# Kernel optimization log

Hardware: AMD Instinct MI355X
Metric: run time of the kernel (lower is better)

## Reference

```python
import jax, jax.numpy as jnp
import numpy as np

NUM_HEADS = 12
KEEP_RATE = 0.7


def setup_inputs() -> dict:
    key = jax.random.key(0)
    ks = jax.random.split(key, 5)
    B, N, C = 64, 197, 768
    x = jax.random.normal(ks[0], (B, N, C), dtype=jnp.float32)
    qkv_w = jax.random.normal(ks[1], (3 * C, C), dtype=jnp.float32) * (C ** -0.5)
    qkv_b = jax.random.normal(ks[2], (3 * C,), dtype=jnp.float32) * 0.02
    proj_w = jax.random.normal(ks[3], (C, C), dtype=jnp.float32) * (C ** -0.5)
    proj_b = jax.random.normal(ks[4], (C,), dtype=jnp.float32) * 0.02
    return {"x": x, "qkv_w": qkv_w, "qkv_b": qkv_b, "proj_w": proj_w, "proj_b": proj_b}


def reference(x, qkv_w, qkv_b, proj_w, proj_b):
    B, N, C = x.shape
    H = NUM_HEADS
    D = C // H
    scale = D ** -0.5
    # qkv projection: [B,N,3C] -> [3,B,H,N,D]
    qkv = (x @ qkv_w.T + qkv_b).reshape(B, N, 3, H, D).transpose(2, 0, 3, 1, 4)
    q, k, v = qkv[0], qkv[1], qkv[2]
    # full materialized attention (required for cls-row extraction)
    attn = jax.nn.softmax(jnp.einsum('bhqd,bhkd->bhqk', q, k) * scale, axis=-1)
    out = jnp.einsum('bhqk,bhkd->bqhd', attn, v).reshape(B, N, C)
    out = out @ proj_w.T + proj_b
    # EViT token pruning: cls-token attention over non-cls keys, head-averaged
    left_tokens = int(KEEP_RATE * (N - 1))  # 137
    cls_attn = attn[:, :, 0, 1:].mean(axis=1)  # [B, N-1]
    _, idx = jax.lax.top_k(cls_attn, left_tokens)  # sorted descending, like torch.topk
    index = jnp.broadcast_to(idx[:, :, None], (B, left_tokens, C))
    return (out, index, idx, cls_attn)
```

## Files before the change

kernel.cpp:

```cpp
#include <hip/hip_runtime.h>
#include <hip/hip_bf16.h>
#include <stdint.h>

constexpr int BATCH = 64;
constexpr int NTOK  = 197;
constexpr int CDIM  = 768;
constexpr int NH    = 12;
constexpr int HD    = 64;
constexpr int MROWS = BATCH * NTOK;
constexpr int MPAD  = 12800;
constexpr int NROWT = MPAD / 128;
constexpr int LEFT  = 137;
constexpr int KPAD  = 224;
constexpr int BH    = BATCH * NH;
constexpr int SPAD  = 208;

constexpr size_t OUT_OFF_OUT   = 0;
constexpr size_t OUT_OFF_INDEX = (size_t)BATCH * NTOK * CDIM;
constexpr size_t OUT_OFF_IDX   = OUT_OFF_INDEX + (size_t)BATCH * LEFT * CDIM;
constexpr size_t OUT_OFF_CLS   = OUT_OFF_IDX + (size_t)BATCH * LEFT;

constexpr size_t WS_CLSPH = 0;
constexpr size_t WS_CLSF  = WS_CLSPH + (size_t)BH * (NTOK - 1);
constexpr size_t WS_IDXI  = WS_CLSF  + (size_t)BATCH * (NTOK - 1);
constexpr size_t WS_Q0    = WS_IDXI  + (size_t)BATCH * LEFT;
constexpr size_t WS_XB    = WS_Q0  + (size_t)BATCH * CDIM;
constexpr size_t WS_WB    = WS_XB  + (size_t)MPAD * CDIM / 2;
constexpr size_t WS_PB    = WS_WB  + (size_t)3 * CDIM * CDIM / 2;
constexpr size_t WS_QB    = WS_PB  + (size_t)CDIM * CDIM / 2;
constexpr size_t WS_KB    = WS_QB  + (size_t)BH * NTOK * HD / 2;
constexpr size_t WS_VTB   = WS_KB  + (size_t)BH * NTOK * HD / 2;
constexpr size_t WS_AOB   = WS_VTB + (size_t)BH * HD * KPAD / 2;
constexpr size_t WS_U     = WS_AOB + (size_t)MPAD * CDIM / 2;
constexpr size_t WS_S     = WS_U   + (size_t)BH * CDIM;

typedef __attribute__((ext_vector_type(8))) short short8;
typedef __attribute__((ext_vector_type(4))) float floatx4;

__device__ __forceinline__ ushort f2bf(float x) {
    __hip_bfloat16 h = __float2bfloat16(x);
    return *(ushort*)&h;
}

__device__ __forceinline__ void load_lds16(const ushort* g, ushort* l) {
    __builtin_amdgcn_global_load_lds(
        (const __attribute__((address_space(1))) uint32_t*)(uintptr_t)g,
        (__attribute__((address_space(3))) uint32_t*)(uint32_t)(uintptr_t)l,
        16, 0, 0);
}

constexpr int X_N4  = MROWS * CDIM / 4;
constexpr int X_NP4 = MPAD * CDIM / 4;
constexpr int W_N4  = 3 * CDIM * CDIM / 4;
constexpr int P_N4  = CDIM * CDIM / 4;
constexpr int CAST_TOTAL = X_NP4 + W_N4 + P_N4;

__global__ __launch_bounds__(256) void cast_all_kernel(const float* __restrict__ x,
                                                       const float* __restrict__ qkv_w,
                                                       const float* __restrict__ proj_w,
                                                       ushort* __restrict__ xb,
                                                       ushort* __restrict__ wb,
                                                       ushort* __restrict__ pb) {
    int i = blockIdx.x * 256 + threadIdx.x;
    const float* src;
    ushort* dst;
    int j, valid;
    if (i < X_NP4) {
        src = x; dst = xb; j = i; valid = (j < X_N4);
    } else if (i < X_NP4 + W_N4) {
        src = qkv_w; dst = wb; j = i - X_NP4; valid = 1;
    } else if (i < CAST_TOTAL) {
        src = proj_w; dst = pb; j = i - X_NP4 - W_N4; valid = 1;
    } else {
        return;
    }
    ushort4 h4 = make_ushort4(0, 0, 0, 0);
    if (valid) {
        float4 a = ((const float4*)src)[j];
        h4 = make_ushort4(f2bf(a.x), f2bf(a.y), f2bf(a.z), f2bf(a.w));
    }
    ((ushort4*)dst)[j] = h4;
}

__global__ __launch_bounds__(256) void q0_kernel(const float* __restrict__ x,
                                                 const float* __restrict__ qkv_w,
                                                 const float* __restrict__ qkv_b,
                                                 float* __restrict__ q0) {
    const int wv   = threadIdx.x >> 6;
    const int lane = threadIdx.x & 63;
    constexpr int CG = CDIM / 4;
    const int b = blockIdx.x / CG;
    const int c = (blockIdx.x - b * CG) * 4 + wv;

    const float* xr = x + (size_t)b * NTOK * CDIM;
    const float* wr = qkv_w + (size_t)c * CDIM;
    float s = 0.f;
#pragma unroll
    for (int i = 0; i < 3; i++) {
        float4 xv = *(const float4*)(xr + lane * 4 + i * 256);
        float4 wv4 = *(const float4*)(wr + lane * 4 + i * 256);
        s += xv.x * wv4.x + xv.y * wv4.y + xv.z * wv4.z + xv.w * wv4.w;
    }
#pragma unroll
    for (int off = 32; off >= 1; off >>= 1) s += __shfl_xor(s, off);
    if (lane == 0) q0[(size_t)b * CDIM + c] = s + qkv_b[c];
}

__global__ __launch_bounds__(256) void u_kernel(const float* __restrict__ q0,
                                                const float* __restrict__ qkv_w,
                                                float* __restrict__ U) {
    const int bh = blockIdx.x;
    const int b  = bh / NH;
    const int h  = bh - b * NH;
    const int t  = threadIdx.x;

    __shared__ float q0s[HD];
    if (t < HD) q0s[t] = q0[(size_t)b * CDIM + h * HD + t];
    __syncthreads();

    const float* wk = qkv_w + (size_t)(CDIM + h * HD) * CDIM;
    float a0 = 0.f, a1 = 0.f, a2 = 0.f;
    for (int d = 0; d < HD; d++) {
        const float qd = q0s[d];
        const float* row = wk + (size_t)d * CDIM;
        a0 = fmaf(qd, row[t],       a0);
        a1 = fmaf(qd, row[t + 256], a1);
        a2 = fmaf(qd, row[t + 512], a2);
    }
    float* ub = U + (size_t)bh * CDIM;
    ub[t] = a0; ub[t + 256] = a1; ub[t + 512] = a2;
}

__global__ __launch_bounds__(256) void score_kernel(const float* __restrict__ x,
                                                    const float* __restrict__ U,
                                                    float* __restrict__ S) {
    const int wv   = threadIdx.x >> 6;
    const int lane = threadIdx.x & 63;
    const int j    = blockIdx.x * 4 + wv;
    const int b    = blockIdx.y;
    if (j >= NTOK) return;

    const float* xr = x + ((size_t)b * NTOK + j) * CDIM;
    float4 xv[3];
#pragma unroll
    for (int i = 0; i < 3; i++) xv[i] = *(const float4*)(xr + lane * 4 + i * 256);

    for (int h = 0; h < NH; h++) {
        const float* ur = U + (size_t)(b * NH + h) * CDIM;
        float s = 0.f;
#pragma unroll
        for (int i = 0; i < 3; i++) {
            float4 uv = *(const float4*)(ur + lane * 4 + i * 256);
            s += xv[i].x * uv.x + xv[i].y * uv.y + xv[i].z * uv.z + xv[i].w * uv.w;
        }
#pragma unroll
        for (int off = 32; off >= 1; off >>= 1) s += __shfl_xor(s, off);
        if (lane == 0) S[(size_t)(b * NH + h) * SPAD + j] = s;
    }
}

template <int MODE, int NCOLT>
__global__ __launch_bounds__(256, 4) void mfma_gemm128(
    const ushort* __restrict__ A, const ushort* __restrict__ W,
    const float* __restrict__ bias,
    float* __restrict__ O0f, ushort* __restrict__ O0q,
    ushort* __restrict__ O1k, ushort* __restrict__ O2vd,
    int Mvalid, int N) {
    constexpr int K   = CDIM;
    constexpr int BK  = 32;
    constexpr int NTK = K / BK;
    __shared__ ushort sA[2 * 128 * BK];
    __shared__ ushort sB[2 * 128 * BK];

    const int t    = threadIdx.x;
    const int lane = t & 63;
    const int w    = t >> 6;
    const int wm   = (w >> 1) * 64;
    const int wn   = (w & 1) * 64;
    const int fr   = lane & 15;
    const int fq   = lane >> 4;
    const int f3   = lane & 3;

    int row, col;
    {
        constexpr int nwg = NROWT * NCOLT;
        constexpr int q = nwg >> 3, r = nwg & 7;
        const int xcd = blockIdx.x & 7, lin = blockIdx.x >> 3;
        const int wg = (xcd < r ? xcd * (q + 1) : r * (q + 1) + (xcd - r) * q) + lin;
        row = wg / NCOLT; col = wg - row * NCOLT;
    }
    const int rowBase = row * 128;
    const int colBase = col * 128;

    auto stage = [&](const ushort* __restrict__ G, ushort* dst, int grow0, int kt) {
#pragma unroll
        for (int i = 0; i < 2; ++i) {
            const int l  = i * 256 + t;
            const int rl = l >> 2;
            const int sl = (l & 3) ^ (rl & 3);
            load_lds16(G + (size_t)(grow0 + rl) * K + kt * BK + sl * 8,
                       dst + l * 8);
        }
    };

    floatx4 acc[4][4];
#pragma unroll
    for (int i = 0; i < 4; ++i)
#pragma unroll
        for (int j = 0; j < 4; ++j)
#pragma unroll
            for (int r2 = 0; r2 < 4; ++r2) acc[i][j][r2] = 0.f;

    const int s0 = (fq ^ f3) * 8;

    stage(A, sA, rowBase, 0);
    stage(W, sB, colBase, 0);

    for (int kt = 0; kt < NTK; ++kt) {
        __syncthreads();
        const int cb = (kt & 1) << 12;
        if (kt + 1 < NTK) {
            stage(A, sA + (cb ^ 4096), rowBase, kt + 1);
            stage(W, sB + (cb ^ 4096), colBase, kt + 1);
        }

        const ushort* pa = sA + cb + (wm + fr) * BK;
        const ushort* pb = sB + cb + (wn + fr) * BK;
        short8 af[4], bf[4];
#pragma unroll
        for (int i = 0; i < 4; ++i) {
            af[i] = *(const short8*)(pa + i * 512 + s0);
            bf[i] = *(const short8*)(pb + i * 512 + s0);
        }
#pragma unroll
        for (int i = 0; i < 4; ++i)
#pragma unroll
            for (int j = 0; j < 4; ++j)
                acc[i][j] = __builtin_amdgcn_mfma_f32_16x16x32_bf16(
                    af[i], bf[j], acc[i][j], 0, 0, 0);
    }

#pragma unroll
    for (int j = 0; j < 4; ++j) {
        const int nn = colBase + wn + j * 16 + fr;
        const float bq = bias[nn];
        if (MODE == 0) {
#pragma unroll
            for (int i = 0; i < 4; ++i) {
                const int mb = rowBase + wm + i * 16 + fq * 4;
#pragma unroll
                for (int r2 = 0; r2 < 4; ++r2) {
                    const int mm = mb + r2;
                    if (mm < Mvalid) O0f[(size_t)mm * N + nn] = acc[i][j][r2] + bq;
                }
            }
        } else {
            const int which = nn / CDIM;
            const int nc    = nn - which * CDIM;
            const int h     = nc >> 6;
            const int d     = nc & 63;
#pragma unroll
            for (int i = 0; i < 4; ++i) {
                const int mb = rowBase + wm + i * 16 + fq * 4;
#pragma unroll
                for (int r2 = 0; r2 < 4; ++r2) {
                    const int mm = mb + r2;
                    if (mm < Mvalid) {
                        const int b   = mm / NTOK;
                        const int tok = mm - b * NTOK;
                        const int bh  = b * NH + h;
                        const ushort val = f2bf(acc[i][j][r2] + bq);
                        if (which == 0)      O0q[((size_t)bh * NTOK + tok) * HD + d] = val;
                        else if (which == 1) O1k[((size_t)bh * NTOK + tok) * HD + d] = val;
                        else                 O2vd[(size_t)mm * CDIM + nc] = val;
                    }
                }
            }
        }
    }
}

__global__ __launch_bounds__(256) void v_transpose_kernel(const ushort* __restrict__ Vd,
                                                          ushort* __restrict__ Vtb) {
    const int bh = blockIdx.x;
    const int b  = bh / NH;
    const int h  = bh - b * NH;
    const int t  = threadIdx.x;

    __shared__ ushort tile[HD][KPAD + 9];

    const int d  = t & 63;
    const int tt = t >> 6;
    const ushort* src = Vd + (size_t)b * NTOK * CDIM + h * HD + d;
    for (int tok0 = 0; tok0 < KPAD; tok0 += 4) {
        const int tok = tok0 + tt;
        ushort v = 0;
        if (tok < NTOK) v = src[(size_t)tok * CDIM];
        tile[d][tok] = v;
    }
    __syncthreads();

    uint* dst = (uint*)(Vtb + (size_t)bh * HD * KPAD);
    constexpr int C2 = KPAD / 2;
    for (int idx = t; idx < HD * C2; idx += 256) {
        const int dd = idx / C2;
        const int c  = idx - dd * C2;
        const uint lo = tile[dd][2 * c];
        const uint hi = tile[dd][2 * c + 1];
        dst[dd * C2 + c] = lo | (hi << 16);
    }
}

__global__ __launch_bounds__(64) void attn_mfma_kernel(const ushort* __restrict__ Qb,
                                                       const ushort* __restrict__ Kb,
                                                       const ushort* __restrict__ Vtb,
                                                       ushort* __restrict__ AOb) {
    const int qt = blockIdx.x;
    const int bh = blockIdx.y;
    const int b  = bh / NH;
    const int h  = bh - b * NH;
    const int lane = threadIdx.x;
    const int qc   = lane & 15;
    const int quad = lane >> 4;

    __shared__ ushort Pl[16][32];
    __shared__ float  alf[16], lf[16];

    const ushort* Qh = Qb  + (size_t)bh * NTOK * HD;
    const ushort* Kh = Kb  + (size_t)bh * NTOK * HD;
    const ushort* Vh = Vtb + (size_t)bh * HD * KPAD;

    const int qrow = min(qt * 16 + qc, NTOK - 1);
    const short8 qf0 = *(const short8*)(Qh + (size_t)qrow * HD + quad * 8);
    const short8 qf1 = *(const short8*)(Qh + (size_t)qrow * HD + 32 + quad * 8);

    floatx4 o[4];
#pragma unroll
    for (int s = 0; s < 4; s++)
#pragma unroll
        for (int r = 0; r < 4; r++) o[s][r] = 0.f;
    float m = -INFINITY, l = 0.f;

    for (int c0 = 0; c0 < NTOK; c0 += 32) {
        const int kr0 = min(c0 + qc, NTOK - 1);
        const int kr1 = min(c0 + 16 + qc, NTOK - 1);
        short8 kf00 = *(const short8*)(Kh + (size_t)kr0 * HD + quad * 8);
        short8 kf01 = *(const short8*)(Kh + (size_t)kr0 * HD + 32 + quad * 8);
        short8 kf10 = *(const short8*)(Kh + (size_t)kr1 * HD + quad * 8);
        short8 kf11 = *(const short8*)(Kh + (size_t)kr1 * HD + 32 + quad * 8);

        floatx4 s0 = {0.f, 0.f, 0.f, 0.f}, s1 = {0.f, 0.f, 0.f, 0.f};
        s0 = __builtin_amdgcn_mfma_f32_16x16x32_bf16(kf00, qf0, s0, 0, 0, 0);
        s0 = __builtin_amdgcn_mfma_f32_16x16x32_bf16(kf01, qf1, s0, 0, 0, 0);
        s1 = __builtin_amdgcn_mfma_f32_16x16x32_bf16(kf10, qf0, s1, 0, 0, 0);
        s1 = __builtin_amdgcn_mfma_f32_16x16x32_bf16(kf11, qf1, s1, 0, 0, 0);

        float sv[8];
        float mloc = -INFINITY;
#pragma unroll
        for (int r = 0; r < 4; r++) {
            const int key0 = c0 + quad * 4 + r;
            const int key1 = key0 + 16;
            sv[r]     = (key0 < NTOK) ? s0[r] * 0.125f : -1e30f;
            sv[4 + r] = (key1 < NTOK) ? s1[r] * 0.125f : -1e30f;
            mloc = fmaxf(mloc, fmaxf(sv[r], sv[4 + r]));
        }
        mloc = fmaxf(mloc, __shfl_xor(mloc, 16));
        mloc = fmaxf(mloc, __shfl_xor(mloc, 32));
        const float mnew  = fmaxf(m, mloc);
        const float alpha = __expf(m - mnew);
        float p[8], ps = 0.f;
#pragma unroll
        for (int i = 0; i < 8; i++) { p[i] = __expf(sv[i] - mnew); ps += p[i]; }
        ps += __shfl_xor(ps, 16);
        ps += __shfl_xor(ps, 32);
        l = l * alpha + ps;
        m = mnew;

#pragma unroll
        for (int r = 0; r < 4; r++) {
            Pl[qc][quad * 4 + r]      = f2bf(p[r]);
            Pl[qc][16 + quad * 4 + r] = f2bf(p[4 + r]);
        }
        if (quad == 0) alf[qc] = alpha;
        __syncthreads();

        float ar[4];
#pragma unroll
        for (int r = 0; r < 4; r++) ar[r] = alf[quad * 4 + r];
#pragma unroll
        for (int s = 0; s < 4; s++)
#pragma unroll
            for (int r = 0; r < 4; r++) o[s][r] *= ar[r];

        const short8 pf = *(const short8*)&Pl[qc][quad * 8];
#pragma unroll
        for (int s = 0; s < 4; s++) {
            const short8 vf = *(const short8*)(Vh + (size_t)(s * 16 + qc) * KPAD + c0 + quad * 8);
            o[s] = __builtin_amdgcn_mfma_f32_16x16x32_bf16(pf, vf, o[s], 0, 0, 0);
        }
        __syncthreads();
    }

    if (quad == 0) lf[qc] = l;
    __syncthreads();

#pragma unroll
    for (int r = 0; r < 4; r++) {
        const int tok = qt * 16 + quad * 4 + r;
        if (tok >= NTOK) continue;
        const float inv = 1.f / lf[quad * 4 + r];
        ushort* dst = AOb + ((size_t)(b * NTOK + tok)) * CDIM + h * HD;
#pragma unroll
        for (int s = 0; s < 4; s++) dst[s * 16 + qc] = f2bf(o[s][r] * inv);
    }
}

__global__ __launch_bounds__(256) void topk_fused_kernel(const float* __restrict__ S,
                                                         const float* __restrict__ q0,
                                                         const float* __restrict__ qkv_b,
                                                         int* __restrict__ idxI,
                                                         float* __restrict__ idxOut,
                                                         float* __restrict__ outCls) {
    const int b    = blockIdx.x;
    const int t    = threadIdx.x;
    const int lane = t & 63;
    const int w    = t >> 6;

    __shared__ float qbv[NH];
    __shared__ float redm[4], reds[4];
    __shared__ float vsh[NTOK - 1];

    if (w == 0) {
        for (int h = 0; h < NH; ++h) {
            float p = q0[(size_t)b * CDIM + h * HD + lane] * qkv_b[CDIM + h * HD + lane];
#pragma unroll
            for (int off = 32; off >= 1; off >>= 1) p += __shfl_xor(p, off);
            if (lane == 0) qbv[h] = p;
        }
    }
    __syncthreads();

    float macc = 0.f;
    for (int h = 0; h < NH; ++h) {
        const float qb = qbv[h];
        const float sv = (t < NTOK) ? (S[(size_t)(b * NH + h) * SPAD + t] + qb) * 0.125f
                                    : -INFINITY;
        float mloc = sv;
#pragma unroll
        for (int off = 32; off >= 1; off >>= 1) mloc = fmaxf(mloc, __shfl_xor(mloc, off));
        if (lane == 0) redm[w] = mloc;
        __syncthreads();
        const float mx = fmaxf(fmaxf(redm[0], redm[1]), fmaxf(redm[2], redm[3]));
        const float p = (t < NTOK) ? expf(sv - mx) : 0.f;
        float ls = p;
#pragma unroll
        for (int off = 32; off >= 1; off >>= 1) ls += __shfl_xor(ls, off);
        if (lane == 0) reds[w] = ls;
        __syncthreads();
        const float denom = (reds[0] + reds[1]) + (reds[2] + reds[3]);
        macc += p / denom;
        __syncthreads();
    }

    if (t >= 1 && t < NTOK) {
        const float val = macc * (1.f / 12.f);
        vsh[t - 1] = val;
        outCls[(size_t)b * (NTOK - 1) + (t - 1)] = val;
    }
    __syncthreads();

    if (t < NTOK - 1) {
        const float vi = vsh[t];
        int rank = 0;
        for (int j = 0; j < NTOK - 1; j++) {
            const float vj = vsh[j];
            rank += (vj > vi) || (vj == vi && j < t);
        }
        if (rank < LEFT) {
            idxI[b * LEFT + rank]   = t;
            idxOut[b * LEFT + rank] = (float)t;
        }
    }
}

__global__ void fill_index_kernel(const int* __restrict__ idxI,
                                  float* __restrict__ dst) {
    int tid = blockIdx.x * 256 + threadIdx.x;
    constexpr int C4 = CDIM / 4;
    if (tid >= BATCH * LEFT * C4) return;
    float v = (float)idxI[tid / C4];
    ((float4*)dst)[tid] = make_float4(v, v, v, v);
}

extern "C" void kernel_launch(void* const* d_in, const int* in_sizes, int n_in,
                              void* d_out, int out_size, void* d_ws, size_t ws_size,
                              hipStream_t stream) {
    const float* x      = (const float*)d_in[0];
    const float* qkv_w  = (const float*)d_in[1];
    const float* qkv_b  = (const float*)d_in[2];
    const float* proj_w = (const float*)d_in[3];
    const float* proj_b = (const float*)d_in[4];
    float* out = (float*)d_out;

    float*  ws    = (float*)d_ws;
    int*    idxi  = (int*)(ws + WS_IDXI);
    float*  q0    = ws + WS_Q0;
    ushort* xb    = (ushort*)(ws + WS_XB);
    ushort* wb    = (ushort*)(ws + WS_WB);
    ushort* pb    = (ushort*)(ws + WS_PB);
    ushort* qb    = (ushort*)(ws + WS_QB);
    ushort* kb    = (ushort*)(ws + WS_KB);
    ushort* vtb   = (ushort*)(ws + WS_VTB);
    ushort* aob   = (ushort*)(ws + WS_AOB);
    ushort* vd    = aob;
    float*  U     = ws + WS_U;
    float*  S     = ws + WS_S;

    cast_all_kernel<<<CAST_TOTAL / 256, 256, 0, stream>>>(x, qkv_w, proj_w, xb, wb, pb);

    q0_kernel<<<BATCH * (CDIM / 4), 256, 0, stream>>>(x, qkv_w, qkv_b, q0);
    u_kernel<<<BH, 256, 0, stream>>>(q0, qkv_w, U);
    score_kernel<<<dim3((NTOK + 3) / 4, BATCH), 256, 0, stream>>>(x, U, S);

    mfma_gemm128<1, 18><<<NROWT * 18, 256, 0, stream>>>(
        xb, wb, qkv_b, nullptr, qb, kb, vd, MROWS, 3 * CDIM);

    v_transpose_kernel<<<BH, 256, 0, stream>>>(vd, vtb);

    attn_mfma_kernel<<<dim3(13, BH), 64, 0, stream>>>(qb, kb, vtb, aob);

    mfma_gemm128<0, 6><<<NROWT * 6, 256, 0, stream>>>(
        aob, pb, proj_b, out + OUT_OFF_OUT, nullptr, nullptr, nullptr,
        MROWS, CDIM);

    topk_fused_kernel<<<BATCH, 256, 0, stream>>>(S, q0, qkv_b, idxi,
                                                 out + OUT_OFF_IDX,
                                                 out + OUT_OFF_CLS);

    fill_index_kernel<<<((size_t)BATCH * LEFT * (CDIM / 4) + 255) / 256, 256, 0, stream>>>(
        idxi, out + OUT_OFF_INDEX);
}
```

Measured before the change: 368.2 us.

## Process four query tiles per attention wave to reuse K/V fragment loads

Each single-wave attention block now handles up to four 16-row query tiles instead of one, so K and V fragments loaded from global memory are shared across four sets of MFMAs. The grid shrinks from 13 to 4 blocks per batch-head, cutting redundant K/V traffic and per-block overhead. In exchange, per-thread register use rises (four accumulator sets and Q fragments), which may lower occupancy. Fewer blocks also means less parallelism, and the last group handles only one tile, leaving work unevenly spread.

```diff
diff --git a/kernel.cpp b/kernel.cpp
--- a/kernel.cpp
+++ b/kernel.cpp
@@ -311,108 +311,142 @@
     }
 }
 
+constexpr int QTPW = 4;
+constexpr int NQG  = 4;
+
 __global__ __launch_bounds__(64) void attn_mfma_kernel(const ushort* __restrict__ Qb,
                                                        const ushort* __restrict__ Kb,
                                                        const ushort* __restrict__ Vtb,
                                                        ushort* __restrict__ AOb) {
-    const int qt = blockIdx.x;
+    const int g  = blockIdx.x;
     const int bh = blockIdx.y;
     const int b  = bh / NH;
     const int h  = bh - b * NH;
     const int lane = threadIdx.x;
     const int qc   = lane & 15;
     const int quad = lane >> 4;
-
-    __shared__ ushort Pl[16][32];
-    __shared__ float  alf[16], lf[16];
+    const int ntv  = min(QTPW, 13 - g * QTPW);
+
+    __shared__ ushort Pl[QTPW][16][32];
+    __shared__ float  alf[QTPW][16], lf[QTPW][16];
 
     const ushort* Qh = Qb  + (size_t)bh * NTOK * HD;
     const ushort* Kh = Kb  + (size_t)bh * NTOK * HD;
     const ushort* Vh = Vtb + (size_t)bh * HD * KPAD;
 
-    const int qrow = min(qt * 16 + qc, NTOK - 1);
-    const short8 qf0 = *(const short8*)(Qh + (size_t)qrow * HD + quad * 8);
-    const short8 qf1 = *(const short8*)(Qh + (size_t)qrow * HD + 32 + quad * 8);
-
-    floatx4 o[4];
-#pragma unroll
-    for (int s = 0; s < 4; s++)
-#pragma unroll
-        for (int r = 0; r < 4; r++) o[s][r] = 0.f;
-    float m = -INFINITY, l = 0.f;
+    short8 qf[QTPW][2];
+#pragma unroll
+    for (int ti = 0; ti < QTPW; ++ti) {
+        if (ti < ntv) {
+            const int qrow = min((g * QTPW + ti) * 16 + qc, NTOK - 1);
+            qf[ti][0] = *(const short8*)(Qh + (size_t)qrow * HD + quad * 8);
+            qf[ti][1] = *(const short8*)(Qh + (size_t)qrow * HD + 32 + quad * 8);
+        }
+    }
+
+    floatx4 o[QTPW][4];
+#pragma unroll
+    for (int ti = 0; ti < QTPW; ++ti)
+#pragma unroll
+        for (int s = 0; s < 4; ++s)
+#pragma unroll
+            for (int r = 0; r < 4; ++r) o[ti][s][r] = 0.f;
+    float m[QTPW], l[QTPW];
+#pragma unroll
+    for (int ti = 0; ti < QTPW; ++ti) { m[ti] = -INFINITY; l[ti] = 0.f; }
 
     for (int c0 = 0; c0 < NTOK; c0 += 32) {
         const int kr0 = min(c0 + qc, NTOK - 1);
         const int kr1 = min(c0 + 16 + qc, NTOK - 1);
-        short8 kf00 = *(const short8*)(Kh + (size_t)kr0 * HD + quad * 8);
-        short8 kf01 = *(const short8*)(Kh + (size_t)kr0 * HD + 32 + quad * 8);
-        short8 kf10 = *(const short8*)(Kh + (size_t)kr1 * HD + quad * 8);
-        short8 kf11 = *(const short8*)(Kh + (size_t)kr1 * HD + 32 + quad * 8);
-
-        floatx4 s0 = {0.f, 0.f, 0.f, 0.f}, s1 = {0.f, 0.f, 0.f, 0.f};
-        s0 = __builtin_amdgcn_mfma_f32_16x16x32_bf16(kf00, qf0, s0, 0, 0, 0);
-        s0 = __builtin_amdgcn_mfma_f32_16x16x32_bf16(kf01, qf1, s0, 0, 0, 0);
-        s1 = __builtin_amdgcn_mfma_f32_16x16x32_bf16(kf10, qf0, s1, 0, 0, 0);
-        s1 = __builtin_amdgcn_mfma_f32_16x16x32_bf16(kf11, qf1, s1, 0, 0, 0);
-
-        float sv[8];
-        float mloc = -INFINITY;
-#pragma unroll
-        for (int r = 0; r < 4; r++) {
-            const int key0 = c0 + quad * 4 + r;
-            const int key1 = key0 + 16;
-            sv[r]     = (key0 < NTOK) ? s0[r] * 0.125f : -1e30f;
-            sv[4 + r] = (key1 < NTOK) ? s1[r] * 0.125f : -1e30f;
-            mloc = fmaxf(mloc, fmaxf(sv[r], sv[4 + r]));
-        }
-        mloc = fmaxf(mloc, __shfl_xor(mloc, 16));
-        mloc = fmaxf(mloc, __shfl_xor(mloc, 32));
-        const float mnew  = fmaxf(m, mloc);
-        const float alpha = __expf(m - mnew);
-        float p[8], ps = 0.f;
-#pragma unroll
-        for (int i = 0; i < 8; i++) { p[i] = __expf(sv[i] - mnew); ps += p[i]; }
-        ps += __shfl_xor(ps, 16);
-        ps += __shfl_xor(ps, 32);
-        l = l * alpha + ps;
-        m = mnew;
-
-#pragma unroll
-        for (int r = 0; r < 4; r++) {
-            Pl[qc][quad * 4 + r]      = f2bf(p[r]);
-            Pl[qc][16 + quad * 4 + r] = f2bf(p[4 + r]);
-        }
-        if (quad == 0) alf[qc] = alpha;
+        const short8 kf00 = *(const short8*)(Kh + (size_t)kr0 * HD + quad * 8);
+        const short8 kf01 = *(const short8*)(Kh + (size_t)kr0 * HD + 32 + quad * 8);
+        const short8 kf10 = *(const short8*)(Kh + (size_t)kr1 * HD + quad * 8);
+        const short8 kf11 = *(const short8*)(Kh + (size_t)kr1 * HD + 32 + quad * 8);
+
+#pragma unroll
+        for (int ti = 0; ti < QTPW; ++ti) {
+            if (ti >= ntv) continue;
+            floatx4 s0 = {0.f, 0.f, 0.f, 0.f}, s1 = {0.f, 0.f, 0.f, 0.f};
+            s0 = __builtin_amdgcn_mfma_f32_16x16x32_bf16(kf00, qf[ti][0], s0, 0, 0, 0);
+            s0 = __builtin_amdgcn_mfma_f32_16x16x32_bf16(kf01, qf[ti][1], s0, 0, 0, 0);
+            s1 = __builtin_amdgcn_mfma_f32_16x16x32_bf16(kf10, qf[ti][0], s1, 0, 0, 0);
+            s1 = __builtin_amdgcn_mfma_f32_16x16x32_bf16(kf11, qf[ti][1], s1, 0, 0, 0);
+
+            float sv[8];
+            float mloc = -INFINITY;
+#pragma unroll
+            for (int r = 0; r < 4; ++r) {
+                const int key0 = c0 + quad * 4 + r;
+                const int key1 = key0 + 16;
+                sv[r]     = (key0 < NTOK) ? s0[r] * 0.125f : -1e30f;
+                sv[4 + r] = (key1 < NTOK) ? s1[r] * 0.125f : -1e30f;
+                mloc = fmaxf(mloc, fmaxf(sv[r], sv[4 + r]));
+            }
+            mloc = fmaxf(mloc, __shfl_xor(mloc, 16));
+            mloc = fmaxf(mloc, __shfl_xor(mloc, 32));
+            const float mnew  = fmaxf(m[ti], mloc);
+            const float alpha = __expf(m[ti] - mnew);
+            float p[8], ps = 0.f;
+#pragma unroll
+            for (int i = 0; i < 8; ++i) { p[i] = __expf(sv[i] - mnew); ps += p[i]; }
+            ps += __shfl_xor(ps, 16);
+            ps += __shfl_xor(ps, 32);
+            l[ti] = l[ti] * alpha + ps;
+            m[ti] = mnew;
+
+#pragma unroll
+            for (int r = 0; r < 4; ++r) {
+                Pl[ti][qc][quad * 4 + r]      = f2bf(p[r]);
+                Pl[ti][qc][16 + quad * 4 + r] = f2bf(p[4 + r]);
+            }
+            if (quad == 0) alf[ti][qc] = alpha;
+        }
         __syncthreads();
 
-        float ar[4];
-#pragma unroll
-        for (int r = 0; r < 4; r++) ar[r] = alf[quad * 4 + r];
-#pragma unroll
-        for (int s = 0; s < 4; s++)
-#pragma unroll
-            for (int r = 0; r < 4; r++) o[s][r] *= ar[r];
-
-        const short8 pf = *(const short8*)&Pl[qc][quad * 8];
-#pragma unroll
-        for (int s = 0; s < 4; s++) {
+        short8 pf[QTPW];
+#pragma unroll
+        for (int ti = 0; ti < QTPW; ++ti) {
+            if (ti >= ntv) continue;
+            pf[ti] = *(const short8*)&Pl[ti][qc][quad * 8];
+            float ar[4];
+#pragma unroll
+            for (int r = 0; r < 4; ++r) ar[r] = alf[ti][quad * 4 + r];
+#pragma unroll
+            for (int s = 0; s < 4; ++s)
+#pragma unroll
+                for (int r = 0; r < 4; ++r) o[ti][s][r] *= ar[r];
+        }
+
+#pragma unroll
+        for (int s = 0; s < 4; ++s) {
             const short8 vf = *(const short8*)(Vh + (size_t)(s * 16 + qc) * KPAD + c0 + quad * 8);
-            o[s] = __builtin_amdgcn_mfma_f32_16x16x32_bf16(pf, vf, o[s], 0, 0, 0);
+#pragma unroll
+            for (int ti = 0; ti < QTPW; ++ti)
+                if (ti < ntv)
+                    o[ti][s] = __builtin_amdgcn_mfma_f32_16x16x32_bf16(
+                        pf[ti], vf, o[ti][s], 0, 0, 0);
         }
         __syncthreads();
     }
 
-    if (quad == 0) lf[qc] = l;
+#pragma unroll
+    for (int ti = 0; ti < QTPW; ++ti)
+        if (ti < ntv && quad == 0) lf[ti][qc] = l[ti];
     __syncthreads();
 
 #pragma unroll
-    for (int r = 0; r < 4; r++) {
-        const int tok = qt * 16 + quad * 4 + r;
-        if (tok >= NTOK) continue;
-        const float inv = 1.f / lf[quad * 4 + r];
-        ushort* dst = AOb + ((size_t)(b * NTOK + tok)) * CDIM + h * HD;
-#pragma unroll
-        for (int s = 0; s < 4; s++) dst[s * 16 + qc] = f2bf(o[s][r] * inv);
+    for (int ti = 0; ti < QTPW; ++ti) {
+        if (ti >= ntv) continue;
+        const int qt = g * QTPW + ti;
+#pragma unroll
+        for (int r = 0; r < 4; ++r) {
+            const int tok = qt * 16 + quad * 4 + r;
+            if (tok >= NTOK) continue;
+            const float inv = 1.f / lf[ti][quad * 4 + r];
+            ushort* dst = AOb + ((size_t)(b * NTOK + tok)) * CDIM + h * HD;
+#pragma unroll
+            for (int s = 0; s < 4; ++s) dst[s * 16 + qc] = f2bf(o[ti][s][r] * inv);
+        }
     }
 }
 
@@ -528,7 +562,7 @@
 
     v_transpose_kernel<<<BH, 256, 0, stream>>>(vd, vtb);
 
-    attn_mfma_kernel<<<dim3(13, BH), 64, 0, stream>>>(qb, kb, vtb, aob);
+    attn_mfma_kernel<<<dim3(NQG, BH), 64, 0, stream>>>(qb, kb, vtb, aob);
 
     mfma_gemm128<0, 6><<<NROWT * 6, 256, 0, stream>>>(
         aob, pb, proj_b, out + OUT_OFF_OUT, nullptr, nullptr, nullptr,
```

Result: faster. 360.2 us (-2.2%).
